# Optimization experiments

Measured on AMD Instinct MI355X. Metric: run time of the kernel, lower is better.

## Reference

```python
import jax, jax.numpy as jnp
import numpy as np

EMB_DIMS = 1024

def setup_inputs() -> dict:
    key = jax.random.key(0)
    k1, k2, k3 = jax.random.split(key, 3)
    B, S, D = 4, 2048, EMB_DIMS
    x = jax.random.normal(k1, (B, S, D), dtype=jnp.float32)
    # nn.Linear(D, 3D): weight stored as [3D, D] in torch; we use [D, 3D] (x @ W)
    w_qkv = jax.random.normal(k2, (D, 3 * D), dtype=jnp.float32) * (D ** -0.5)
    b_qkv = jax.random.normal(k3, (3 * D,), dtype=jnp.float32) * 0.01
    return {"x": x, "w_qkv": w_qkv, "b_qkv": b_qkv}

def reference(x, w_qkv, b_qkv):
    D = x.shape[-1]
    scale = D ** (-0.5)  # torch code divides qk by this (i.e. multiplies by sqrt(D))
    qkv = x @ w_qkv + b_qkv                      # [B,S,3D]
    q, k, v = jnp.split(qkv, 3, axis=-1)         # each [B,S,D]
    scores = jnp.einsum('bsd,btd->bst', q, k) / scale  # [B,S,S]
    attn = jax.nn.sigmoid(scores)                # sigmoid, NOT softmax
    return jnp.einsum('bst,btd->bsd', attn, v)   # [B,S,D]
```

## Files before the change

kernel.cpp:

```cpp
#include <hip/hip_runtime.h>
#include <stdint.h>

typedef unsigned short u16;
typedef _Float16 f16x8 __attribute__((ext_vector_type(8)));
typedef float f32x4 __attribute__((ext_vector_type(4)));

#define B_   4
#define S_   2048
#define D_   1024
#define ND3  3072

__device__ __forceinline__ u16 f2h(float x) {
    union { _Float16 h; u16 u; } v; v.h = (_Float16)x; return v.u;
}

__device__ __forceinline__ void gload_lds16(const u16* g, u16* l) {
    __builtin_amdgcn_global_load_lds((const __attribute__((address_space(1))) void*)g,
                                     (__attribute__((address_space(3))) void*)l, 16, 0, 0);
}

__device__ __forceinline__ int xcd_swz(int lid, int nwg) {
    int c = nwg >> 3;
    return (lid & 7) * c + (lid >> 3);
}

template<int NT>
__device__ __forceinline__ void gemm_wide(const u16* __restrict__ A, const u16* __restrict__ Bt,
                                          int lda, int ldb, int rowbase, int colbase,
                                          u16* ldsA, u16* ldsB, f32x4 (&acc)[4][4])
{
    const int NSTEP = 2 * NT;
    const int tid  = threadIdx.x;
    const int lane = tid & 63;
    const int w    = tid >> 6;
    const int wr   = w >> 2, wc = w & 3;

    const int r0 = tid >> 2;
    const int c0 = (((tid & 3) ^ ((tid >> 3) & 3)) << 3);
    const uint32_t offA0 = (uint32_t)(rowbase + r0) * lda + c0;
    const uint32_t offB0 = (uint32_t)(colbase + r0) * ldb + c0;
    const uint32_t offB1 = offB0 + (uint32_t)128 * ldb;
    const int dst = tid << 3;

    const int rd_lane = ((lane & 15) << 5) + ((((lane >> 4) ^ (lane >> 1)) & 3) << 3);
    const int wrOff = wr << 11;
    const int wcOff = wc << 11;

#define ISSUE(sv) do { int s_ = (sv); \
    if (s_ < NSTEP) { \
        uint32_t ko_ = (uint32_t)s_ << 5; \
        int st_ = s_ % 3; \
        int slA_ = st_ << 12;              \
        int slB_ = st_ << 13;              \
        gload_lds16(A  + offA0 + ko_, ldsA + slA_ + dst); \
        gload_lds16(Bt + offB0 + ko_, ldsB + slB_ + dst); \
        gload_lds16(Bt + offB1 + ko_, ldsB + slB_ + dst + 4096); \
    } } while (0)

    f16x8 af[4], bf[4];

    ISSUE(0); ISSUE(1);
    int sl = 0;
    for (int S = 0; S < NSTEP; ++S) {
        asm volatile("s_waitcnt lgkmcnt(0)" ::: "memory");
        if (S < NSTEP - 1) asm volatile("s_waitcnt vmcnt(3)" ::: "memory");
        else               asm volatile("s_waitcnt vmcnt(0)" ::: "memory");
        __builtin_amdgcn_s_barrier();
        asm volatile("" ::: "memory");
        ISSUE(S + 2);
        const int slA = sl << 12, slB = sl << 13;
#pragma unroll
        for (int mq = 0; mq < 4; ++mq)
            af[mq] = *(const f16x8*)(ldsA + slA + wrOff + (mq << 9) + rd_lane);
#pragma unroll
        for (int n = 0; n < 4; ++n)
            bf[n] = *(const f16x8*)(ldsB + slB + wcOff + (n << 9) + rd_lane);
#pragma unroll
        for (int mq = 0; mq < 4; ++mq)
#pragma unroll
            for (int n = 0; n < 4; ++n)
                acc[mq][n] = __builtin_amdgcn_mfma_f32_16x16x32_f16(af[mq], bf[n], acc[mq][n], 0, 0, 0);
        sl = (sl == 2) ? 0 : sl + 1;
    }
#undef ISSUE
}

template<int NT>
__device__ __forceinline__ void gemm_narrow(const u16* __restrict__ A, const u16* __restrict__ Bt,
                                            int lda, int ldb, int rowbase, int colbase,
                                            u16* ldsA, u16* ldsB, f32x4 (&acc)[4][2])
{
    const int NSTEP = 2 * NT;
    const int tid  = threadIdx.x;
    const int lane = tid & 63;
    const int w    = tid >> 6;
    const int wr   = w >> 2, wc = w & 3;

    const int r0 = tid >> 2;
    const int c0 = (((tid & 3) ^ ((tid >> 3) & 3)) << 3);
    const uint32_t offA0 = (uint32_t)(rowbase + r0) * lda + c0;
    const uint32_t offB0 = (uint32_t)(colbase + r0) * ldb + c0;
    const int dst = tid << 3;

    const int rd_lane = ((lane & 15) << 5) + ((((lane >> 4) ^ (lane >> 1)) & 3) << 3);
    const int wrOff = wr << 11;
    const int wcOff = wc << 10;

#define ISSUE(sv) do { int s_ = (sv); \
    if (s_ < NSTEP) { \
        uint32_t ko_ = (uint32_t)s_ << 5; \
        int sl_ = (s_ % 3) << 12; \
        gload_lds16(A  + offA0 + ko_, ldsA + sl_ + dst); \
        gload_lds16(Bt + offB0 + ko_, ldsB + sl_ + dst); \
    } } while (0)

    f16x8 af[4], bf[2];

    ISSUE(0); ISSUE(1);
    int sl = 0;
    for (int S = 0; S < NSTEP; ++S) {
        asm volatile("s_waitcnt lgkmcnt(0)" ::: "memory");
        if (S < NSTEP - 1) asm volatile("s_waitcnt vmcnt(2)" ::: "memory");
        else               asm volatile("s_waitcnt vmcnt(0)" ::: "memory");
        __builtin_amdgcn_s_barrier();
        asm volatile("" ::: "memory");
        ISSUE(S + 2);
        const int slo = sl << 12;
#pragma unroll
        for (int mq = 0; mq < 4; ++mq)
            af[mq] = *(const f16x8*)(ldsA + slo + wrOff + (mq << 9) + rd_lane);
#pragma unroll
        for (int n = 0; n < 2; ++n)
            bf[n] = *(const f16x8*)(ldsB + slo + wcOff + (n << 9) + rd_lane);
#pragma unroll
        for (int mq = 0; mq < 4; ++mq)
#pragma unroll
            for (int n = 0; n < 2; ++n)
                acc[mq][n] = __builtin_amdgcn_mfma_f32_16x16x32_f16(af[mq], bf[n], acc[mq][n], 0, 0, 0);
        sl = (sl == 2) ? 0 : sl + 1;
    }
#undef ISSUE
}

__global__ __launch_bounds__(256) void k_cvt_f16(const float* __restrict__ in,
                                                 u16* __restrict__ oh, int n) {
    int i = (blockIdx.x * 256 + threadIdx.x) << 3;
    if (i >= n) return;
    float4 a = *(const float4*)(in + i);
    float4 b = *(const float4*)(in + i + 4);
    ushort4 h0, h1;
    h0.x = f2h(a.x); h0.y = f2h(a.y); h0.z = f2h(a.z); h0.w = f2h(a.w);
    h1.x = f2h(b.x); h1.y = f2h(b.y); h1.z = f2h(b.z); h1.w = f2h(b.w);
    *(ushort4*)(oh + i)     = h0;
    *(ushort4*)(oh + i + 4) = h1;
}

__global__ __launch_bounds__(256) void k_transpose_f16(const float* __restrict__ W,
                                                       u16* __restrict__ Wt, int R, int C) {
    __shared__ float t[32][33];
    int tx = threadIdx.x & 31, ty = threadIdx.x >> 5;
    int c0 = blockIdx.x << 5, r0 = blockIdx.y << 5;
#pragma unroll
    for (int i = 0; i < 4; ++i) {
        int r = (i << 3) + ty;
        t[r][tx] = W[(size_t)(r0 + r) * C + c0 + tx];
    }
    __syncthreads();
#pragma unroll
    for (int i = 0; i < 4; ++i) {
        int r = (i << 3) + ty;
        Wt[(size_t)(c0 + r) * R + r0 + tx] = f2h(t[tx][r]);
    }
}

__global__ __launch_bounds__(512, 4) void k_qkv(const u16* __restrict__ xh,
                                                const u16* __restrict__ wt,
                                                const float* __restrict__ bias,
                                                u16* __restrict__ qf, u16* __restrict__ kf,
                                                u16* __restrict__ vt) {
    __shared__ u16 lds[36864];
    f32x4 acc[4][4];
    f32x4 z = {0.f, 0.f, 0.f, 0.f};
#pragma unroll
    for (int m = 0; m < 4; ++m)
#pragma unroll
        for (int n = 0; n < 4; ++n) acc[m][n] = z;

    const int lid = blockIdx.y * 12 + blockIdx.x;
    const int swz = xcd_swz(lid, 768);
    const int bx = swz % 12, by = swz / 12;
    const int rowbase = by << 7;
    const int colbase = bx << 8;
    gemm_wide<16>(xh, wt, D_, D_, rowbase, colbase, lds, lds + 12288, acc);

    const int lane = threadIdx.x & 63;
    const int w = threadIdx.x >> 6;
    const int wr = w >> 2, wc = w & 3;
    const int region = colbase >> 10;
#pragma unroll
    for (int m = 0; m < 4; ++m) {
        int gr0 = rowbase + wr * 64 + m * 16 + ((lane >> 4) << 2);
#pragma unroll
        for (int n = 0; n < 4; ++n) {
            int gc = colbase + wc * 64 + n * 16 + (lane & 15);
            float bv = bias[gc];
            if (region == 0) {
#pragma unroll
                for (int r = 0; r < 4; ++r)
                    qf[(size_t)(gr0 + r) * D_ + gc] = f2h(acc[m][n][r] + bv);
            } else if (region == 1) {
                int c = gc - 1024;
#pragma unroll
                for (int r = 0; r < 4; ++r)
                    kf[(size_t)(gr0 + r) * D_ + c] = f2h(acc[m][n][r] + bv);
            } else {
                int d  = gc - 2048;
                int b  = gr0 >> 11;
                int t0 = gr0 & 2047;
                size_t base = (((size_t)b << 10) + d) * (size_t)S_ + t0;
#pragma unroll
                for (int r = 0; r < 4; ++r)
                    vt[base + r] = f2h(acc[m][n][r] + bv);
            }
        }
    }
}

__global__ __launch_bounds__(512, 4) void k_scores(const u16* __restrict__ qf,
                                                   const u16* __restrict__ kf,
                                                   u16* __restrict__ attn) {
    __shared__ u16 lds[36864];
    f32x4 acc[4][4];
    f32x4 z = {0.f, 0.f, 0.f, 0.f};
#pragma unroll
    for (int m = 0; m < 4; ++m)
#pragma unroll
        for (int n = 0; n < 4; ++n) acc[m][n] = z;

    const int m_ = (blockIdx.z << 4) + blockIdx.y;
    const int P  = (blockIdx.x << 3) + (m_ >> 3);
    const int bx = m_ & 7, by = P & 15, b = P >> 4;

    const size_t boff = (size_t)b * S_ * D_;
    u16* att = attn + (size_t)b * S_ * S_;
    const int rowbase = by << 7, colbase = bx << 8;
    gemm_wide<16>(qf + boff, kf + boff, D_, D_, rowbase, colbase, lds, lds + 12288, acc);

    const int lane = threadIdx.x & 63;
    const int w = threadIdx.x >> 6;
    const int wr = w >> 2, wc = w & 3;
#pragma unroll
    for (int m = 0; m < 4; ++m) {
        int gr0 = rowbase + wr * 64 + m * 16 + ((lane >> 4) << 2);
#pragma unroll
        for (int n = 0; n < 4; ++n) {
            int gc = colbase + wc * 64 + n * 16 + (lane & 15);
#pragma unroll
            for (int r = 0; r < 4; ++r) {
                float sv = acc[m][n][r] * 32.0f;
                float sg = 1.0f / (1.0f + __expf(-sv));
                att[(size_t)(gr0 + r) * S_ + gc] = f2h(sg);
            }
        }
    }
}

__global__ __launch_bounds__(512, 4) void k_pv(const u16* __restrict__ attn,
                                               const u16* __restrict__ vt,
                                               float* __restrict__ out) {
    __shared__ u16 lds[24576];
    f32x4 acc[4][2];
    f32x4 z = {0.f, 0.f, 0.f, 0.f};
#pragma unroll
    for (int m = 0; m < 4; ++m)
#pragma unroll
        for (int n = 0; n < 2; ++n) acc[m][n] = z;

    const int m_ = (blockIdx.z << 4) + blockIdx.y;
    const int P  = (blockIdx.x << 3) + (m_ >> 3);
    const int bx = m_ & 7, by = P & 15, b = P >> 4;

    const u16* Aa = attn + (size_t)b * S_ * S_;
    const u16* Bv = vt   + (size_t)b * D_ * S_;
    float* ob     = out  + (size_t)b * S_ * D_;
    const int rowbase = by << 7, colbase = bx << 7;
    gemm_narrow<32>(Aa, Bv, S_, S_, rowbase, colbase, lds, lds + 12288, acc);

    const int lane = threadIdx.x & 63;
    const int w = threadIdx.x >> 6;
    const int wr = w >> 2, wc = w & 3;
#pragma unroll
    for (int m = 0; m < 4; ++m) {
        int gr0 = rowbase + wr * 64 + m * 16 + ((lane >> 4) << 2);
#pragma unroll
        for (int n = 0; n < 2; ++n) {
            int gc = colbase + wc * 32 + n * 16 + (lane & 15);
#pragma unroll
            for (int r = 0; r < 4; ++r)
                ob[(size_t)(gr0 + r) * D_ + gc] = acc[m][n][r];
        }
    }
}

extern "C" void kernel_launch(void* const* d_in, const int* in_sizes, int n_in,
                              void* d_out, int out_size, void* d_ws, size_t ws_size,
                              hipStream_t stream) {
    const float* x    = (const float*)d_in[0];
    const float* wqkv = (const float*)d_in[1];
    const float* bias = (const float*)d_in[2];
    float* out = (float*)d_out;

    const size_t MB = 1048576;
    uint8_t* ws = (uint8_t*)d_ws;
    u16* xh   = (u16*)(ws);
    u16* wt   = (u16*)(ws + 16 * MB);
    u16* qf   = (u16*)(ws + 32 * MB);
    u16* kf   = (u16*)(ws + 48 * MB);
    u16* vt   = (u16*)(ws + 64 * MB);
    u16* attn = (u16*)(ws);

    k_cvt_f16<<<dim3(4096), dim3(256), 0, stream>>>(x, xh, B_ * S_ * D_);
    k_transpose_f16<<<dim3(ND3 / 32, D_ / 32), dim3(256), 0, stream>>>(wqkv, wt, D_, ND3);
    k_qkv<<<dim3(ND3 / 256, (B_ * S_) / 128), dim3(512), 0, stream>>>(xh, wt, bias, qf, kf, vt);
    k_scores<<<dim3(S_ / 256, S_ / 128, B_), dim3(512), 0, stream>>>(qf, kf, attn);
    k_pv<<<dim3(D_ / 128, S_ / 128, B_), dim3(512), 0, stream>>>(attn, vt, out);
}
```

Before: 160.8 us.

## Widen PV GEMM tiles to 128x256 and merge prep kernels into one launch

The P·V kernel now uses the wide 128x256 GEMM path with XCD-swizzled block mapping instead of the narrow 128x128 path. This halves how often the attention matrix is re-read and gives more MFMA work per LDS load, at the cost of more accumulator registers, more LDS, and only 256 blocks. The fp32→fp16 conversion of x and the weight transpose are combined into one launch to save a kernel launch gap.

```diff
diff --git a/kernel.cpp b/kernel.cpp
--- a/kernel.cpp
+++ b/kernel.cpp
@@ -50,8 +50,8 @@
     if (s_ < NSTEP) { \
         uint32_t ko_ = (uint32_t)s_ << 5; \
         int st_ = s_ % 3; \
-        int slA_ = st_ << 12;              \
-        int slB_ = st_ << 13;              \
+        int slA_ = st_ << 12; \
+        int slB_ = st_ << 13; \
         gload_lds16(A  + offA0 + ko_, ldsA + slA_ + dst); \
         gload_lds16(Bt + offB0 + ko_, ldsB + slB_ + dst); \
         gload_lds16(Bt + offB1 + ko_, ldsB + slB_ + dst + 4096); \
@@ -85,91 +85,35 @@
 #undef ISSUE
 }
 
-template<int NT>
-__device__ __forceinline__ void gemm_narrow(const u16* __restrict__ A, const u16* __restrict__ Bt,
-                                            int lda, int ldb, int rowbase, int colbase,
-                                            u16* ldsA, u16* ldsB, f32x4 (&acc)[4][2])
-{
-    const int NSTEP = 2 * NT;
-    const int tid  = threadIdx.x;
-    const int lane = tid & 63;
-    const int w    = tid >> 6;
-    const int wr   = w >> 2, wc = w & 3;
-
-    const int r0 = tid >> 2;
-    const int c0 = (((tid & 3) ^ ((tid >> 3) & 3)) << 3);
-    const uint32_t offA0 = (uint32_t)(rowbase + r0) * lda + c0;
-    const uint32_t offB0 = (uint32_t)(colbase + r0) * ldb + c0;
-    const int dst = tid << 3;
-
-    const int rd_lane = ((lane & 15) << 5) + ((((lane >> 4) ^ (lane >> 1)) & 3) << 3);
-    const int wrOff = wr << 11;
-    const int wcOff = wc << 10;
-
-#define ISSUE(sv) do { int s_ = (sv); \
-    if (s_ < NSTEP) { \
-        uint32_t ko_ = (uint32_t)s_ << 5; \
-        int sl_ = (s_ % 3) << 12; \
-        gload_lds16(A  + offA0 + ko_, ldsA + sl_ + dst); \
-        gload_lds16(Bt + offB0 + ko_, ldsB + sl_ + dst); \
-    } } while (0)
-
-    f16x8 af[4], bf[2];
-
-    ISSUE(0); ISSUE(1);
-    int sl = 0;
-    for (int S = 0; S < NSTEP; ++S) {
-        asm volatile("s_waitcnt lgkmcnt(0)" ::: "memory");
-        if (S < NSTEP - 1) asm volatile("s_waitcnt vmcnt(2)" ::: "memory");
-        else               asm volatile("s_waitcnt vmcnt(0)" ::: "memory");
-        __builtin_amdgcn_s_barrier();
-        asm volatile("" ::: "memory");
-        ISSUE(S + 2);
-        const int slo = sl << 12;
-#pragma unroll
-        for (int mq = 0; mq < 4; ++mq)
-            af[mq] = *(const f16x8*)(ldsA + slo + wrOff + (mq << 9) + rd_lane);
-#pragma unroll
-        for (int n = 0; n < 2; ++n)
-            bf[n] = *(const f16x8*)(ldsB + slo + wcOff + (n << 9) + rd_lane);
-#pragma unroll
-        for (int mq = 0; mq < 4; ++mq)
-#pragma unroll
-            for (int n = 0; n < 2; ++n)
-                acc[mq][n] = __builtin_amdgcn_mfma_f32_16x16x32_f16(af[mq], bf[n], acc[mq][n], 0, 0, 0);
-        sl = (sl == 2) ? 0 : sl + 1;
-    }
-#undef ISSUE
-}
-
-__global__ __launch_bounds__(256) void k_cvt_f16(const float* __restrict__ in,
-                                                 u16* __restrict__ oh, int n) {
-    int i = (blockIdx.x * 256 + threadIdx.x) << 3;
-    if (i >= n) return;
-    float4 a = *(const float4*)(in + i);
-    float4 b = *(const float4*)(in + i + 4);
-    ushort4 h0, h1;
-    h0.x = f2h(a.x); h0.y = f2h(a.y); h0.z = f2h(a.z); h0.w = f2h(a.w);
-    h1.x = f2h(b.x); h1.y = f2h(b.y); h1.z = f2h(b.z); h1.w = f2h(b.w);
-    *(ushort4*)(oh + i)     = h0;
-    *(ushort4*)(oh + i + 4) = h1;
-}
-
-__global__ __launch_bounds__(256) void k_transpose_f16(const float* __restrict__ W,
-                                                       u16* __restrict__ Wt, int R, int C) {
+__global__ __launch_bounds__(256) void k_prep(const float* __restrict__ x, u16* __restrict__ xh,
+                                              const float* __restrict__ W, u16* __restrict__ Wt) {
     __shared__ float t[32][33];
-    int tx = threadIdx.x & 31, ty = threadIdx.x >> 5;
-    int c0 = blockIdx.x << 5, r0 = blockIdx.y << 5;
-#pragma unroll
-    for (int i = 0; i < 4; ++i) {
-        int r = (i << 3) + ty;
-        t[r][tx] = W[(size_t)(r0 + r) * C + c0 + tx];
-    }
-    __syncthreads();
-#pragma unroll
-    for (int i = 0; i < 4; ++i) {
-        int r = (i << 3) + ty;
-        Wt[(size_t)(c0 + r) * R + r0 + tx] = f2h(t[tx][r]);
+    int bb = blockIdx.x;
+    if (bb < 4096) {
+        int i = (bb * 256 + threadIdx.x) << 3;
+        if (i >= B_ * S_ * D_) return;
+        float4 a = *(const float4*)(x + i);
+        float4 b = *(const float4*)(x + i + 4);
+        ushort4 h0, h1;
+        h0.x = f2h(a.x); h0.y = f2h(a.y); h0.z = f2h(a.z); h0.w = f2h(a.w);
+        h1.x = f2h(b.x); h1.y = f2h(b.y); h1.z = f2h(b.z); h1.w = f2h(b.w);
+        *(ushort4*)(xh + i)     = h0;
+        *(ushort4*)(xh + i + 4) = h1;
+    } else {
+        bb -= 4096;
+        int c0 = (bb % 96) << 5, r0 = (bb / 96) << 5;
+        int tx = threadIdx.x & 31, ty = threadIdx.x >> 5;
+#pragma unroll
+        for (int i = 0; i < 4; ++i) {
+            int r = (i << 3) + ty;
+            t[r][tx] = W[(size_t)(r0 + r) * ND3 + c0 + tx];
+        }
+        __syncthreads();
+#pragma unroll
+        for (int i = 0; i < 4; ++i) {
+            int r = (i << 3) + ty;
+            Wt[(size_t)(c0 + r) * D_ + r0 + tx] = f2h(t[tx][r]);
+        }
     }
 }
 
@@ -268,23 +212,23 @@
 __global__ __launch_bounds__(512, 4) void k_pv(const u16* __restrict__ attn,
                                                const u16* __restrict__ vt,
                                                float* __restrict__ out) {
-    __shared__ u16 lds[24576];
-    f32x4 acc[4][2];
+    __shared__ u16 lds[36864];
+    f32x4 acc[4][4];
     f32x4 z = {0.f, 0.f, 0.f, 0.f};
 #pragma unroll
     for (int m = 0; m < 4; ++m)
 #pragma unroll
-        for (int n = 0; n < 2; ++n) acc[m][n] = z;
-
-    const int m_ = (blockIdx.z << 4) + blockIdx.y;
-    const int P  = (blockIdx.x << 3) + (m_ >> 3);
-    const int bx = m_ & 7, by = P & 15, b = P >> 4;
+        for (int n = 0; n < 4; ++n) acc[m][n] = z;
+
+    const int lid = (blockIdx.z << 6) + (blockIdx.y << 2) + blockIdx.x;
+    const int swz = xcd_swz(lid, 256);
+    const int bx = swz & 3, by = (swz >> 2) & 15, b = swz >> 6;
 
     const u16* Aa = attn + (size_t)b * S_ * S_;
     const u16* Bv = vt   + (size_t)b * D_ * S_;
     float* ob     = out  + (size_t)b * S_ * D_;
-    const int rowbase = by << 7, colbase = bx << 7;
-    gemm_narrow<32>(Aa, Bv, S_, S_, rowbase, colbase, lds, lds + 12288, acc);
+    const int rowbase = by << 7, colbase = bx << 8;
+    gemm_wide<32>(Aa, Bv, S_, S_, rowbase, colbase, lds, lds + 12288, acc);
 
     const int lane = threadIdx.x & 63;
     const int w = threadIdx.x >> 6;
@@ -293,8 +237,8 @@
     for (int m = 0; m < 4; ++m) {
         int gr0 = rowbase + wr * 64 + m * 16 + ((lane >> 4) << 2);
 #pragma unroll
-        for (int n = 0; n < 2; ++n) {
-            int gc = colbase + wc * 32 + n * 16 + (lane & 15);
+        for (int n = 0; n < 4; ++n) {
+            int gc = colbase + wc * 64 + n * 16 + (lane & 15);
 #pragma unroll
             for (int r = 0; r < 4; ++r)
                 ob[(size_t)(gr0 + r) * D_ + gc] = acc[m][n][r];
@@ -319,9 +263,8 @@
     u16* vt   = (u16*)(ws + 64 * MB);
     u16* attn = (u16*)(ws);
 
-    k_cvt_f16<<<dim3(4096), dim3(256), 0, stream>>>(x, xh, B_ * S_ * D_);
-    k_transpose_f16<<<dim3(ND3 / 32, D_ / 32), dim3(256), 0, stream>>>(wqkv, wt, D_, ND3);
+    k_prep<<<dim3(4096 + 3072), dim3(256), 0, stream>>>(x, xh, wqkv, wt);
     k_qkv<<<dim3(ND3 / 256, (B_ * S_) / 128), dim3(512), 0, stream>>>(xh, wt, bias, qf, kf, vt);
     k_scores<<<dim3(S_ / 256, S_ / 128, B_), dim3(512), 0, stream>>>(qf, kf, attn);
-    k_pv<<<dim3(D_ / 128, S_ / 128, B_), dim3(512), 0, stream>>>(attn, vt, out);
-}
+    k_pv<<<dim3(D_ / 256, S_ / 128, B_), dim3(512), 0, stream>>>(attn, vt, out);
+}
```

Measured after the change: 156.8 us (median of 2 runs). 1.03x faster.
